# Kernel optimization log

Measured on AMD Instinct MI355X. Metric: run time of the kernel, lower is better.

The kernel has to match this reference:

```python
import jax, jax.numpy as jnp
import numpy as np

N_NODES = 50000
N_EDGES = 800000
IN_CH = 256
OUT_CH = 64
HEADS = 4
NEG_SLOPE = 0.2


def setup_inputs() -> dict:
    key = jax.random.key(0)
    k = jax.random.split(key, 7)
    x = jax.random.normal(k[0], (N_NODES, IN_CH), dtype=jnp.float32)
    edge_index = jax.random.randint(k[1], (2, N_EDGES), 0, N_NODES, dtype=jnp.int32)
    # Glorot-style init for the linear projection and attention vectors
    W = jax.random.normal(k[2], (IN_CH, HEADS * OUT_CH), dtype=jnp.float32) / np.sqrt(IN_CH)
    att_src = jax.random.normal(k[3], (HEADS, OUT_CH), dtype=jnp.float32) / np.sqrt(OUT_CH)
    att_dst = jax.random.normal(k[4], (HEADS, OUT_CH), dtype=jnp.float32) / np.sqrt(OUT_CH)
    bias = jnp.zeros((HEADS * OUT_CH,), dtype=jnp.float32)
    return {"x": x, "edge_index": edge_index, "W": W,
            "att_src": att_src, "att_dst": att_dst, "bias": bias}


def reference(x, edge_index, W, att_src, att_dst, bias):
    N = x.shape[0]
    # PyG GATConv default: add self-loops
    loop = jnp.arange(N, dtype=edge_index.dtype)
    src = jnp.concatenate([edge_index[0], loop])
    dst = jnp.concatenate([edge_index[1], loop])

    h = (x @ W).reshape(N, HEADS, OUT_CH)          # [N,H,C]
    a_src = jnp.einsum('nhc,hc->nh', h, att_src)    # [N,H]
    a_dst = jnp.einsum('nhc,hc->nh', h, att_dst)    # [N,H]

    alpha = a_src[src] + a_dst[dst]                 # [E,H]
    alpha = jax.nn.leaky_relu(alpha, NEG_SLOPE)

    # segment softmax over edges grouped by destination node
    amax = jax.ops.segment_max(alpha, dst, num_segments=N)
    amax = jnp.where(jnp.isfinite(amax), amax, 0.0)
    e = jnp.exp(alpha - amax[dst])
    denom = jax.ops.segment_sum(e, dst, num_segments=N)
    coef = e / (denom[dst] + 1e-16)                 # [E,H]

    msg = coef[..., None] * h[src]                  # [E,H,C]
    out = jax.ops.segment_sum(msg, dst, num_segments=N)  # [N,H,C]
    out = out.reshape(N, HEADS * OUT_CH) + bias
    return jax.nn.relu(out)
```

## Files before the change

### kernel.cpp

```cpp
#include <hip/hip_runtime.h>
#include <hip/hip_bf16.h>

#define HC 256
#define NEG_SLOPE 0.2f
#define BM 64
#define LDKF 264

typedef short short8_t __attribute__((ext_vector_type(8)));
typedef float float4_t __attribute__((ext_vector_type(4)));
typedef int   int4_t   __attribute__((ext_vector_type(4)));

__device__ __forceinline__ unsigned short f2bf(float f) {
  unsigned u = __float_as_uint(f);
  return (unsigned short)((u + 0x7fffu + ((u >> 16) & 1u)) >> 16);
}
__device__ __forceinline__ float bf2f(unsigned short b) {
  return __uint_as_float(((unsigned)b) << 16);
}

__global__ void wt_kernel(const float* __restrict__ W, unsigned short* __restrict__ Wt,
                          int* __restrict__ deg, int n)
{
  const int k = blockIdx.x;
  const int t = threadIdx.x;
  Wt[t * 256 + k] = f2bf(W[k * 256 + t]);
  const int i = k * 256 + t;
  if (i < n) deg[i] = 0;
}

__global__ __launch_bounds__(256) void gemm_mfma(
    const float* __restrict__ x, const unsigned short* __restrict__ Wt,
    const float* __restrict__ att_src, const float* __restrict__ att_dst,
    unsigned short* __restrict__ h, float* __restrict__ a_src,
    float* __restrict__ a_dst, int nnodes)
{
  __shared__ unsigned short As[BM * LDKF];
  const int t    = threadIdx.x;
  const int wv   = t >> 6;
  const int lane = t & 63;
  const int r0   = blockIdx.x * BM;

  {
    const int row = t >> 2, kcb = (t & 3) * 16;
    const int gr = r0 + row;
    #pragma unroll
    for (int k0 = 0; k0 < 256; k0 += 64) {
      float4 xv[4];
      if (gr < nnodes) {
        const float4* p = (const float4*)(x + (size_t)gr * 256 + k0 + kcb);
        xv[0] = p[0]; xv[1] = p[1]; xv[2] = p[2]; xv[3] = p[3];
      } else {
        xv[0] = xv[1] = xv[2] = xv[3] = make_float4(0.f, 0.f, 0.f, 0.f);
      }
      const float* f = (const float*)xv;
      unsigned pk[8];
      #pragma unroll
      for (int i = 0; i < 8; ++i) {
        __hip_bfloat162 b2 = __float22bfloat162_rn(make_float2(f[2 * i], f[2 * i + 1]));
        pk[i] = *(unsigned*)&b2;
      }
      uint4* d = (uint4*)&As[row * LDKF + k0 + kcb];
      d[0] = make_uint4(pk[0], pk[1], pk[2], pk[3]);
      d[1] = make_uint4(pk[4], pk[5], pk[6], pk[7]);
    }
  }
  __syncthreads();

  const int l15 = lane & 15, q = lane >> 4;
  float4_t acc[4][4] = {};

  const unsigned short* __restrict__ Bp = Wt + ((size_t)(64 * wv + l15)) * 256 + q * 8;

  #pragma unroll
  for (int kstep = 0; kstep < 8; ++kstep) {
    const int ko = kstep * 32;
    short8_t bfr[4], af[4];
    #pragma unroll
    for (int nt = 0; nt < 4; ++nt)
      bfr[nt] = *(const short8_t*)(Bp + nt * 16 * 256 + ko);
    #pragma unroll
    for (int mt = 0; mt < 4; ++mt)
      af[mt] = *(const short8_t*)&As[(16 * mt + l15) * LDKF + ko + q * 8];
    #pragma unroll
    for (int mt = 0; mt < 4; ++mt)
      #pragma unroll
      for (int nt = 0; nt < 4; ++nt)
        acc[mt][nt] = __builtin_amdgcn_mfma_f32_16x16x32_bf16(
            af[mt], bfr[nt], acc[mt][nt], 0, 0, 0);
  }

  float atts[4], attd[4];
  #pragma unroll
  for (int nt = 0; nt < 4; ++nt) {
    atts[nt] = att_src[wv * 64 + 16 * nt + l15];
    attd[nt] = att_dst[wv * 64 + 16 * nt + l15];
  }

  #pragma unroll
  for (int mt = 0; mt < 4; ++mt) {
    #pragma unroll
    for (int reg = 0; reg < 4; ++reg) {
      const int row = r0 + 16 * mt + 4 * q + reg;
      const bool ok = row < nnodes;
      float ps = 0.f, pd = 0.f;
      #pragma unroll
      for (int nt = 0; nt < 4; ++nt) {
        const float v = acc[mt][nt][reg];
        if (ok) h[(size_t)row * 256 + 64 * wv + 16 * nt + l15] = f2bf(v);
        ps += v * atts[nt];
        pd += v * attd[nt];
      }
      #pragma unroll
      for (int off = 8; off; off >>= 1) {
        ps += __shfl_down(ps, off, 16);
        pd += __shfl_down(pd, off, 16);
      }
      if (ok && l15 == 0) {
        a_src[row * 4 + wv] = ps;
        a_dst[row * 4 + wv] = pd;
      }
    }
  }
}

__global__ void deg_count(const int* __restrict__ ei, int* __restrict__ deg, int E)
{
  const int e = blockIdx.x * blockDim.x + threadIdx.x;
  if (e >= E) return;
  atomicAdd(&deg[ei[E + e]], 1);
}

__global__ __launch_bounds__(256) void scan_p1(const int* __restrict__ deg,
                                               int* __restrict__ bsum, int n)
{
  __shared__ int ws[4];
  const int t = threadIdx.x, lane = t & 63, wv = t >> 6;
  const int base = blockIdx.x * 1024 + t * 4;
  int4 v = make_int4(0, 0, 0, 0);
  if (base + 3 < n) v = *(const int4*)&deg[base];
  else {
    if (base + 0 < n) v.x = deg[base + 0];
    if (base + 1 < n) v.y = deg[base + 1];
    if (base + 2 < n) v.z = deg[base + 2];
  }
  int s = (v.x + v.y) + (v.z + v.w);
  #pragma unroll
  for (int off = 32; off; off >>= 1) s += __shfl_down(s, off, 64);
  if (lane == 0) ws[wv] = s;
  __syncthreads();
  if (t == 0) bsum[blockIdx.x] = (ws[0] + ws[1]) + (ws[2] + ws[3]);
}

__global__ __launch_bounds__(1024) void scan_p2(const int* __restrict__ bsum,
                                                int* __restrict__ boff,
                                                int* __restrict__ rowptr,
                                                int nb, int n)
{
  __shared__ int wsum[16], woff[16];
  const int t = threadIdx.x, lane = t & 63, wv = t >> 6;
  int v = (t < nb) ? bsum[t] : 0;
  int sc = v;
  #pragma unroll
  for (int off = 1; off < 64; off <<= 1) {
    int u = __shfl_up(sc, off, 64);
    if (lane >= off) sc += u;
  }
  if (lane == 63) wsum[wv] = sc;
  __syncthreads();
  if (t == 0) {
    int run = 0;
    #pragma unroll
    for (int i = 0; i < 16; ++i) { int x = wsum[i]; woff[i] = run; run += x; }
    rowptr[n] = run;
  }
  __syncthreads();
  if (t < nb) boff[t] = woff[wv] + sc - v;
}

__global__ __launch_bounds__(256) void scan_p3(const int* __restrict__ deg,
                                               const int* __restrict__ boff,
                                               int* __restrict__ rowptr,
                                               int* __restrict__ cursor, int n)
{
  __shared__ int wsum[4], woff[4];
  const int t = threadIdx.x, lane = t & 63, wv = t >> 6;
  const int base = blockIdx.x * 1024 + t * 4;
  int4 v = make_int4(0, 0, 0, 0);
  if (base + 3 < n) v = *(const int4*)&deg[base];
  else {
    if (base + 0 < n) v.x = deg[base + 0];
    if (base + 1 < n) v.y = deg[base + 1];
    if (base + 2 < n) v.z = deg[base + 2];
  }
  const int s = (v.x + v.y) + (v.z + v.w);
  int sc = s;
  #pragma unroll
  for (int off = 1; off < 64; off <<= 1) {
    int u = __shfl_up(sc, off, 64);
    if (lane >= off) sc += u;
  }
  if (lane == 63) wsum[wv] = sc;
  __syncthreads();
  if (t == 0) {
    int run = 0;
    #pragma unroll
    for (int i = 0; i < 4; ++i) { int x = wsum[i]; woff[i] = run; run += x; }
  }
  __syncthreads();
  int excl = boff[blockIdx.x] + woff[wv] + (sc - s);
  int4 r;
  r.x = excl;
  r.y = r.x + v.x;
  r.z = r.y + v.y;
  r.w = r.z + v.z;
  if (base + 3 < n) {
    *(int4*)&rowptr[base] = r;
    *(int4*)&cursor[base] = r;
  } else {
    if (base + 0 < n) { rowptr[base + 0] = r.x; cursor[base + 0] = r.x; }
    if (base + 1 < n) { rowptr[base + 1] = r.y; cursor[base + 1] = r.y; }
    if (base + 2 < n) { rowptr[base + 2] = r.z; cursor[base + 2] = r.z; }
  }
}

__global__ __launch_bounds__(256) void fill_csr(
    const int* __restrict__ ei, int* __restrict__ cursor,
    int* __restrict__ csr_src, int E, int nnodes)
{
  const int g    = blockIdx.x & 7;
  const int bg   = blockIdx.x >> 3;
  const int nbg  = gridDim.x >> 3;
  const int gsz  = (nnodes + 7) >> 3;
  const int dlo  = g * gsz;
  const int dhi  = min(dlo + gsz, nnodes);

  for (int e = bg * 256 + threadIdx.x; e < E; e += nbg * 256) {
    const int d = ei[E + e];
    if (d < dlo || d >= dhi) continue;
    const int pos = atomicAdd(&cursor[d], 1);
    csr_src[pos] = ei[e];
  }
}

__device__ __forceinline__ float4 ld_h(const unsigned short* __restrict__ h,
                                       int row, int cb)
{
  const ushort4 u = *(const ushort4*)&h[(size_t)row * 256 + cb];
  return make_float4(bf2f(u.x), bf2f(u.y), bf2f(u.z), bf2f(u.w));
}

__device__ __forceinline__ float edge_w(float as, float ad)
{
  float al = as + ad;
  al = al > 0.f ? al : NEG_SLOPE * al;
  return expf(al);
}

__global__ __launch_bounds__(256) void gather_kernel(
    const int* __restrict__ rowptr, const int* __restrict__ csr_src,
    const unsigned short* __restrict__ h,
    const float* __restrict__ a_src, const float* __restrict__ a_dst,
    const float* __restrict__ bias, float* __restrict__ out, int n)
{
  const int wave = threadIdx.x >> 6;
  const int lane = threadIdx.x & 63;
  const int d = blockIdx.x * 4 + wave;
  if (d >= n) return;

  const int head = lane >> 4;
  const int cb   = lane * 4;

  const float ad = a_dst[d * 4 + head];

  const float w = edge_w(a_src[d * 4 + head], ad);
  float dsum = w;
  float4 hv = ld_h(h, d, cb);
  float4 acc = make_float4(w * hv.x, w * hv.y, w * hv.z, w * hv.w);

  int j = rowptr[d];
  const int end = rowptr[d + 1];

  int4_t sC = {0, 0, 0, 0};
  if (j + 3 < end)
    sC = __builtin_nontemporal_load((const int4_t*)&csr_src[j]);
  while (j + 3 < end) {
    const int jn = j + 4;
    const int jp = (jn + 3 < end) ? jn : j;
    const int4_t sN = __builtin_nontemporal_load((const int4_t*)&csr_src[jp]);

    const float as0 = a_src[sC.x * 4 + head];
    const float as1 = a_src[sC.y * 4 + head];
    const float as2 = a_src[sC.z * 4 + head];
    const float as3 = a_src[sC.w * 4 + head];
    const float4 h0 = ld_h(h, sC.x, cb);
    const float4 h1 = ld_h(h, sC.y, cb);
    const float4 h2 = ld_h(h, sC.z, cb);
    const float4 h3 = ld_h(h, sC.w, cb);

    const float w0 = edge_w(as0, ad);
    const float w1 = edge_w(as1, ad);
    const float w2 = edge_w(as2, ad);
    const float w3 = edge_w(as3, ad);

    dsum += (w0 + w1) + (w2 + w3);
    acc.x += w0 * h0.x + w1 * h1.x + w2 * h2.x + w3 * h3.x;
    acc.y += w0 * h0.y + w1 * h1.y + w2 * h2.y + w3 * h3.y;
    acc.z += w0 * h0.z + w1 * h1.z + w2 * h2.z + w3 * h3.z;
    acc.w += w0 * h0.w + w1 * h1.w + w2 * h2.w + w3 * h3.w;

    sC = sN; j = jn;
  }
  for (; j < end; ++j) {
    const int s0 = csr_src[j];
    const float w0 = edge_w(a_src[s0 * 4 + head], ad);
    const float4 h0 = ld_h(h, s0, cb);
    dsum += w0;
    acc.x += w0 * h0.x; acc.y += w0 * h0.y;
    acc.z += w0 * h0.z; acc.w += w0 * h0.w;
  }

  const float inv = 1.f / (dsum + 1e-16f);
  const float4 b4 = ((const float4*)bias)[lane];
  float4 o;
  o.x = acc.x * inv + b4.x; o.x = o.x > 0.f ? o.x : 0.f;
  o.y = acc.y * inv + b4.y; o.y = o.y > 0.f ? o.y : 0.f;
  o.z = acc.z * inv + b4.z; o.z = o.z > 0.f ? o.z : 0.f;
  o.w = acc.w * inv + b4.w; o.w = o.w > 0.f ? o.w : 0.f;
  *(float4*)&out[(size_t)d * 256 + cb] = o;
}

extern "C" void kernel_launch(void* const* d_in, const int* in_sizes, int n_in,
                              void* d_out, int out_size, void* d_ws, size_t ws_size,
                              hipStream_t stream)
{
  const float* x       = (const float*)d_in[0];
  const int*   ei      = (const int*)d_in[1];
  const float* W       = (const float*)d_in[2];
  const float* att_src = (const float*)d_in[3];
  const float* att_dst = (const float*)d_in[4];
  const float* bias    = (const float*)d_in[5];

  const int nnodes = in_sizes[0] / HC;
  const int E      = in_sizes[1] / 2;
  const int nb     = (nnodes + 1023) / 1024;

  float* out = (float*)d_out;
  char* ws = (char*)d_ws;
  unsigned short* h  = (unsigned short*)ws;
  float* a_src = (float*)(ws + (size_t)nnodes * HC * 2);
  float* a_dst = a_src + (size_t)nnodes * 4;
  unsigned short* Wt = (unsigned short*)(a_dst + (size_t)nnodes * 4);
  int* deg    = (int*)((char*)Wt + 256 * 256 * 2);
  int* rowptr = deg + nnodes;
  int* cursor = rowptr + ((nnodes + 1 + 3) & ~3);
  int* bsum   = cursor + nnodes;
  int* boff   = bsum + ((nb + 3) & ~3);
  int* csr    = boff + ((nb + 3) & ~3);

  wt_kernel<<<256, 256, 0, stream>>>(W, Wt, deg, nnodes);

  gemm_mfma<<<(nnodes + BM - 1) / BM, 256, 0, stream>>>(
      x, Wt, att_src, att_dst, h, a_src, a_dst, nnodes);

  deg_count<<<(E + 255) / 256, 256, 0, stream>>>(ei, deg, E);
  scan_p1<<<nb, 256, 0, stream>>>(deg, bsum, nnodes);
  scan_p2<<<1, 1024, 0, stream>>>(bsum, boff, rowptr, nb, nnodes);
  scan_p3<<<nb, 256, 0, stream>>>(deg, boff, rowptr, cursor, nnodes);

  fill_csr<<<1024, 256, 0, stream>>>(ei, cursor, csr, E, nnodes);

  gather_kernel<<<(nnodes + 3) / 4, 256, 0, stream>>>(
      rowptr, csr, h, a_src, a_dst, bias, out, nnodes);
}
```

Baseline: 279.9 us.

## Fuse degree counting into GEMM launch and collapse scan into one block

Degree-count atomics now run as extra blocks appended to the GEMM grid, so they share one launch and overlap with the GEMM work. The three-kernel prefix scan becomes a single 1024-thread block in which each thread serially sums about 49 degrees. This removes three launches and the inter-kernel gaps. The cost is a serial single-block scan with strided, uncoalesced per-thread loads, and atomic traffic that competes with the GEMM.

After: 370.9 us. +32.5%, slower.

```diff
diff --git a/kernel.cpp b/kernel.cpp
--- a/kernel.cpp
+++ b/kernel.cpp
@@ -28,14 +28,23 @@
   if (i < n) deg[i] = 0;
 }
 
-__global__ __launch_bounds__(256) void gemm_mfma(
+__global__ __launch_bounds__(256) void gemm_deg(
     const float* __restrict__ x, const unsigned short* __restrict__ Wt,
     const float* __restrict__ att_src, const float* __restrict__ att_dst,
     unsigned short* __restrict__ h, float* __restrict__ a_src,
-    float* __restrict__ a_dst, int nnodes)
+    float* __restrict__ a_dst, int nnodes,
+    const int* __restrict__ ei, int* __restrict__ deg, int E, int NG, int ND)
 {
   __shared__ unsigned short As[BM * LDKF];
-  const int t    = threadIdx.x;
+  const int t = threadIdx.x;
+
+  if (blockIdx.x >= NG) {
+    const int b = blockIdx.x - NG;
+    for (int e = b * 256 + t; e < E; e += ND * 256)
+      atomicAdd(&deg[ei[E + e]], 1);
+    return;
+  }
+
   const int wv   = t >> 6;
   const int lane = t & 63;
   const int r0   = blockIdx.x * BM;
@@ -123,76 +132,18 @@
   }
 }
 
-__global__ void deg_count(const int* __restrict__ ei, int* __restrict__ deg, int E)
-{
-  const int e = blockIdx.x * blockDim.x + threadIdx.x;
-  if (e >= E) return;
-  atomicAdd(&deg[ei[E + e]], 1);
-}
-
-__global__ __launch_bounds__(256) void scan_p1(const int* __restrict__ deg,
-                                               int* __restrict__ bsum, int n)
-{
-  __shared__ int ws[4];
-  const int t = threadIdx.x, lane = t & 63, wv = t >> 6;
-  const int base = blockIdx.x * 1024 + t * 4;
-  int4 v = make_int4(0, 0, 0, 0);
-  if (base + 3 < n) v = *(const int4*)&deg[base];
-  else {
-    if (base + 0 < n) v.x = deg[base + 0];
-    if (base + 1 < n) v.y = deg[base + 1];
-    if (base + 2 < n) v.z = deg[base + 2];
-  }
-  int s = (v.x + v.y) + (v.z + v.w);
-  #pragma unroll
-  for (int off = 32; off; off >>= 1) s += __shfl_down(s, off, 64);
-  if (lane == 0) ws[wv] = s;
-  __syncthreads();
-  if (t == 0) bsum[blockIdx.x] = (ws[0] + ws[1]) + (ws[2] + ws[3]);
-}
-
-__global__ __launch_bounds__(1024) void scan_p2(const int* __restrict__ bsum,
-                                                int* __restrict__ boff,
-                                                int* __restrict__ rowptr,
-                                                int nb, int n)
+__global__ __launch_bounds__(1024) void scan_all(
+    const int* __restrict__ deg, int* __restrict__ rowptr,
+    int* __restrict__ cursor, int n)
 {
   __shared__ int wsum[16], woff[16];
   const int t = threadIdx.x, lane = t & 63, wv = t >> 6;
-  int v = (t < nb) ? bsum[t] : 0;
-  int sc = v;
-  #pragma unroll
-  for (int off = 1; off < 64; off <<= 1) {
-    int u = __shfl_up(sc, off, 64);
-    if (lane >= off) sc += u;
-  }
-  if (lane == 63) wsum[wv] = sc;
-  __syncthreads();
-  if (t == 0) {
-    int run = 0;
-    #pragma unroll
-    for (int i = 0; i < 16; ++i) { int x = wsum[i]; woff[i] = run; run += x; }
-    rowptr[n] = run;
-  }
-  __syncthreads();
-  if (t < nb) boff[t] = woff[wv] + sc - v;
-}
-
-__global__ __launch_bounds__(256) void scan_p3(const int* __restrict__ deg,
-                                               const int* __restrict__ boff,
-                                               int* __restrict__ rowptr,
-                                               int* __restrict__ cursor, int n)
-{
-  __shared__ int wsum[4], woff[4];
-  const int t = threadIdx.x, lane = t & 63, wv = t >> 6;
-  const int base = blockIdx.x * 1024 + t * 4;
-  int4 v = make_int4(0, 0, 0, 0);
-  if (base + 3 < n) v = *(const int4*)&deg[base];
-  else {
-    if (base + 0 < n) v.x = deg[base + 0];
-    if (base + 1 < n) v.y = deg[base + 1];
-    if (base + 2 < n) v.z = deg[base + 2];
-  }
-  const int s = (v.x + v.y) + (v.z + v.w);
+  const int C = (n + 1023) / 1024;
+  const int lo = t * C, hi = min(lo + C, n);
+
+  int s = 0;
+  for (int i = lo; i < hi; ++i) s += deg[i];
+
   int sc = s;
   #pragma unroll
   for (int off = 1; off < 64; off <<= 1) {
@@ -204,22 +155,16 @@
   if (t == 0) {
     int run = 0;
     #pragma unroll
-    for (int i = 0; i < 4; ++i) { int x = wsum[i]; woff[i] = run; run += x; }
+    for (int i = 0; i < 16; ++i) { int x = wsum[i]; woff[i] = run; run += x; }
+    rowptr[n] = run;
   }
   __syncthreads();
-  int excl = boff[blockIdx.x] + woff[wv] + (sc - s);
-  int4 r;
-  r.x = excl;
-  r.y = r.x + v.x;
-  r.z = r.y + v.y;
-  r.w = r.z + v.z;
-  if (base + 3 < n) {
-    *(int4*)&rowptr[base] = r;
-    *(int4*)&cursor[base] = r;
-  } else {
-    if (base + 0 < n) { rowptr[base + 0] = r.x; cursor[base + 0] = r.x; }
-    if (base + 1 < n) { rowptr[base + 1] = r.y; cursor[base + 1] = r.y; }
-    if (base + 2 < n) { rowptr[base + 2] = r.z; cursor[base + 2] = r.z; }
+
+  int run = woff[wv] + (sc - s);
+  for (int i = lo; i < hi; ++i) {
+    const int dg = deg[i];
+    rowptr[i] = run; cursor[i] = run;
+    run += dg;
   }
 }
 
@@ -342,7 +287,6 @@
 
   const int nnodes = in_sizes[0] / HC;
   const int E      = in_sizes[1] / 2;
-  const int nb     = (nnodes + 1023) / 1024;
 
   float* out = (float*)d_out;
   char* ws = (char*)d_ws;
@@ -353,19 +297,17 @@
   int* deg    = (int*)((char*)Wt + 256 * 256 * 2);
   int* rowptr = deg + nnodes;
   int* cursor = rowptr + ((nnodes + 1 + 3) & ~3);
-  int* bsum   = cursor + nnodes;
-  int* boff   = bsum + ((nb + 3) & ~3);
-  int* csr    = boff + ((nb + 3) & ~3);
+  int* csr    = cursor + ((nnodes + 3) & ~3);
+
+  const int NG = (nnodes + BM - 1) / BM;
+  const int ND = 1024;
 
   wt_kernel<<<256, 256, 0, stream>>>(W, Wt, deg, nnodes);
 
-  gemm_mfma<<<(nnodes + BM - 1) / BM, 256, 0, stream>>>(
-      x, Wt, att_src, att_dst, h, a_src, a_dst, nnodes);
-
-  deg_count<<<(E + 255) / 256, 256, 0, stream>>>(ei, deg, E);
-  scan_p1<<<nb, 256, 0, stream>>>(deg, bsum, nnodes);
-  scan_p2<<<1, 1024, 0, stream>>>(bsum, boff, rowptr, nb, nnodes);
-  scan_p3<<<nb, 256, 0, stream>>>(deg, boff, rowptr, cursor, nnodes);
+  gemm_deg<<<NG + ND, 256, 0, stream>>>(
+      x, Wt, att_src, att_dst, h, a_src, a_dst, nnodes, ei, deg, E, NG, ND);
+
+  scan_all<<<1, 1024, 0, stream>>>(deg, rowptr, cursor, nnodes);
 
   fill_csr<<<1024, 256, 0, stream>>>(ei, cursor, csr, E, nnodes);
 
```
